# Optimization experiments

Measured on AMD Instinct MI355X. Metric: run time of the kernel, lower is better.

The kernel has to match this reference:

```python
import jax, jax.numpy as jnp
import numpy as np

EMB = 768
HEADS = 12
B, N = 8, 1024


def setup_inputs() -> dict:
    key = jax.random.key(0)
    ks = jax.random.split(key, 5)
    x = jax.random.normal(ks[0], (B, N, EMB), dtype=jnp.float32)
    # torch Linear params expressed as (in, out) matrices: y = x @ W + b
    W_qkv = jax.random.normal(ks[1], (EMB, 3 * EMB), dtype=jnp.float32) * (EMB ** -0.5)
    b_qkv = jax.random.normal(ks[2], (3 * EMB,), dtype=jnp.float32) * 0.02
    W_proj = jax.random.normal(ks[3], (EMB, EMB), dtype=jnp.float32) * (EMB ** -0.5)
    b_proj = jax.random.normal(ks[4], (EMB,), dtype=jnp.float32) * 0.02
    return {"x": x, "W_qkv": W_qkv, "b_qkv": b_qkv, "W_proj": W_proj, "b_proj": b_proj}


def reference(x, W_qkv, b_qkv, W_proj, b_proj):
    b, n, e = x.shape
    h = HEADS
    d = e // h
    qkv = x @ W_qkv + b_qkv                      # (b, n, 3e)
    # rearrange 'b n (h d qkv) -> qkv b h n d': qkv is the INNERMOST factor
    qkv = qkv.reshape(b, n, h, d, 3)
    q = jnp.transpose(qkv[..., 0], (0, 2, 1, 3))  # (b, h, n, d)
    k = jnp.transpose(qkv[..., 1], (0, 2, 1, 3))
    v = jnp.transpose(qkv[..., 2], (0, 2, 1, 3))
    energy = jnp.einsum('bhqd,bhkd->bhqk', q, k)  # UNscaled scores
    # faithful to source: softmax first, THEN divide by sqrt(emb_size)
    att = jax.nn.softmax(energy, axis=-1) / jnp.sqrt(jnp.float32(e))
    out = jnp.einsum('bhql,bhld->bhqd', att, v)   # (b, h, n, d)
    out = jnp.transpose(out, (0, 2, 1, 3)).reshape(b, n, e)
    return out @ W_proj + b_proj
```

## Files before the change

kernel.cpp:

```cpp
#include <hip/hip_runtime.h>
#include <hip/hip_bf16.h>
#include <stdint.h>

#define EMB 768
#define HEADS 12
#define BATCH 8
#define SEQ 1024
#define HD 64
#define M_ROWS (BATCH * SEQ)
#define QKV_COLS (3 * EMB)

typedef __attribute__((ext_vector_type(8))) short short8;
typedef __attribute__((ext_vector_type(4))) float f32x4;

__device__ __forceinline__ unsigned short f2bf(float x) {
    union { float f; unsigned u; } v; v.f = x;
    unsigned r = v.u + 0x7FFFu + ((v.u >> 16) & 1u);
    return (unsigned short)(r >> 16);
}
__device__ __forceinline__ float bf2f(unsigned short h) {
    union { unsigned u; float f; } v; v.u = ((unsigned)h) << 16;
    return v.f;
}
__device__ __forceinline__ float truncbf(float x) {
    return __uint_as_float(__float_as_uint(x) & 0xFFFF0000u);
}
__device__ __forceinline__ uint32_t packtr(float a, float b) {
    return (__float_as_uint(a) >> 16) | (__float_as_uint(b) & 0xFFFF0000u);
}

#define MFMA16(a, b, c) __builtin_amdgcn_mfma_f32_16x16x32_bf16((a), (b), (c), 0, 0, 0)

__global__ __launch_bounds__(256, 2)
void gemm_qkv(const float* __restrict__ X, const float* __restrict__ W,
              const float* __restrict__ bias,
              unsigned short* __restrict__ Qh, unsigned short* __restrict__ Ql,
              unsigned short* __restrict__ Kh, unsigned short* __restrict__ Kl,
              unsigned short* __restrict__ Vt)
{
    __shared__ unsigned short Ash[128][40], Asl[128][40];
    __shared__ unsigned short Bsh[128][40], Bsl[128][40];

    const int tid  = threadIdx.x;
    const int wave = tid >> 6, lane = tid & 63;
    const int lr = lane & 15, lg = lane >> 4;
    const int wr = (wave >> 1) * 64, wc = (wave & 1) * 64;
    const int m0 = blockIdx.y * 128;
    const int c0 = blockIdx.x * 128;

    const f32x4 fzero = {0.f, 0.f, 0.f, 0.f};
    f32x4 acc[4][4];
    #pragma unroll
    for (int m = 0; m < 4; ++m)
        #pragma unroll
        for (int n = 0; n < 4; ++n) acc[m][n] = fzero;

    const int kgB = tid & 7;
    const int cgB = tid >> 3;

    for (int k0 = 0; k0 < EMB; k0 += 32) {
        #pragma unroll
        for (int p = 0; p < 4; ++p) {
            int idx = (p << 8) + tid;
            int row = idx >> 3, kc = (idx & 7) << 2;
            f32x4 v = *reinterpret_cast<const f32x4*>(X + (size_t)(m0 + row) * EMB + k0 + kc);
            float l0 = v[0] - truncbf(v[0]), l1 = v[1] - truncbf(v[1]);
            float l2 = v[2] - truncbf(v[2]), l3 = v[3] - truncbf(v[3]);
            uint2 hw = { packtr(v[0], v[1]), packtr(v[2], v[3]) };
            uint2 lw = { packtr(l0, l1), packtr(l2, l3) };
            *reinterpret_cast<uint2*>(&Ash[row][kc]) = hw;
            *reinterpret_cast<uint2*>(&Asl[row][kc]) = lw;
        }
        {
            f32x4 v[4];
            #pragma unroll
            for (int i = 0; i < 4; ++i)
                v[i] = *reinterpret_cast<const f32x4*>(
                    W + (size_t)(k0 + kgB * 4 + i) * QKV_COLS + c0 + cgB * 4);
            #pragma unroll
            for (int j = 0; j < 4; ++j) {
                float a0 = v[0][j], a1 = v[1][j], a2 = v[2][j], a3 = v[3][j];
                float b0 = a0 - truncbf(a0), b1 = a1 - truncbf(a1);
                float b2 = a2 - truncbf(a2), b3 = a3 - truncbf(a3);
                uint2 hw = { packtr(a0, a1), packtr(a2, a3) };
                uint2 lw = { packtr(b0, b1), packtr(b2, b3) };
                *reinterpret_cast<uint2*>(&Bsh[cgB * 4 + j][kgB * 4]) = hw;
                *reinterpret_cast<uint2*>(&Bsl[cgB * 4 + j][kgB * 4]) = lw;
            }
        }
        __syncthreads();

        short8 ah[4], al[4], bh[4], bl[4];
        #pragma unroll
        for (int m = 0; m < 4; ++m) {
            ah[m] = *reinterpret_cast<const short8*>(&Ash[wr + m * 16 + lr][lg << 3]);
            al[m] = *reinterpret_cast<const short8*>(&Asl[wr + m * 16 + lr][lg << 3]);
        }
        #pragma unroll
        for (int n = 0; n < 4; ++n) {
            bh[n] = *reinterpret_cast<const short8*>(&Bsh[wc + n * 16 + lr][lg << 3]);
            bl[n] = *reinterpret_cast<const short8*>(&Bsl[wc + n * 16 + lr][lg << 3]);
        }
        #pragma unroll
        for (int m = 0; m < 4; ++m)
            #pragma unroll
            for (int n = 0; n < 4; ++n) {
                acc[m][n] = MFMA16(ah[m], bh[n], acc[m][n]);
                acc[m][n] = MFMA16(ah[m], bl[n], acc[m][n]);
                acc[m][n] = MFMA16(al[m], bh[n], acc[m][n]);
            }
        __syncthreads();
    }

    #pragma unroll
    for (int m = 0; m < 4; ++m) {
        #pragma unroll
        for (int n = 0; n < 4; ++n) {
            const int colg = c0 + wc + n * 16 + lr;
            const float bv = bias[colg];
            const int which = colg % 3;
            const int h  = colg / 192;
            const int dd = (colg % 192) / 3;
            const int rowg0 = m0 + wr + m * 16 + (lg << 2);
            const int bi = rowg0 >> 10, ni0 = rowg0 & (SEQ - 1);
            const int bhid = bi * HEADS + h;
            if (which == 2) {
                const float v0 = acc[m][n][0] + bv, v1 = acc[m][n][1] + bv;
                const float v2 = acc[m][n][2] + bv, v3 = acc[m][n][3] + bv;
                uint2 w = { (uint32_t)f2bf(v0) | ((uint32_t)f2bf(v1) << 16),
                            (uint32_t)f2bf(v2) | ((uint32_t)f2bf(v3) << 16) };
                *reinterpret_cast<uint2*>(Vt + ((size_t)bhid * HD + dd) * SEQ + ni0) = w;
            } else {
                unsigned short* __restrict__ Ph = (which == 0) ? Qh : Kh;
                unsigned short* __restrict__ Pl = (which == 0) ? Ql : Kl;
                #pragma unroll
                for (int j = 0; j < 4; ++j) {
                    const float val = acc[m][n][j] + bv;
                    const size_t oidx = ((size_t)bhid * SEQ + ni0 + j) * HD + dd;
                    const uint32_t uv = __float_as_uint(val);
                    Ph[oidx] = (unsigned short)(uv >> 16);
                    Pl[oidx] = (unsigned short)(__float_as_uint(
                        val - __uint_as_float(uv & 0xFFFF0000u)) >> 16);
                }
            }
        }
    }
}

__global__ __launch_bounds__(256, 2)
void attn_fused(const unsigned short* __restrict__ Qh, const unsigned short* __restrict__ Ql,
                const unsigned short* __restrict__ Kh, const unsigned short* __restrict__ Kl,
                const unsigned short* __restrict__ Vt,
                unsigned short* __restrict__ Ob)
{
    __shared__ unsigned short Vs[64][72];
    __shared__ unsigned short Ksh[64][72];
    __shared__ unsigned short Ksl[64][72];
    __shared__ unsigned short Plds[4][16][72];

    const int tid  = threadIdx.x;
    const int wave = tid >> 6, lane = tid & 63;
    const int lr = lane & 15, lg = lane >> 4;

    const int bid = blockIdx.x;
    const int lid = (bid & 7) * 192 + (bid >> 3);
    const int qt = lid & 15;
    const int bh = lid >> 4;
    const int b = bh / HEADS, h = bh % HEADS;

    const size_t base = (size_t)bh * SEQ * HD;
    const unsigned short* Qhb = Qh + base;
    const unsigned short* Qlb = Ql + base;
    const unsigned short* Khb = Kh + base;
    const unsigned short* Klb = Kl + base;
    const unsigned short* Vtb = Vt + base;

    const int q0 = qt * 64 + wave * 16;

    short8 qh[2], ql[2];
    #pragma unroll
    for (int kk = 0; kk < 2; ++kk) {
        const size_t off = (size_t)(q0 + lr) * HD + kk * 32 + (lg << 3);
        qh[kk] = *reinterpret_cast<const short8*>(Qhb + off);
        ql[kk] = *reinterpret_cast<const short8*>(Qlb + off);
    }

    float m = -1.0e30f, l = 0.f;
    f32x4 oacc[4];
    const f32x4 fzero = {0.f, 0.f, 0.f, 0.f};
    #pragma unroll
    for (int d = 0; d < 4; ++d) oacc[d] = fzero;

    for (int t = 0; t < SEQ / 64; ++t) {
        const int kbase = t * 64;

        __syncthreads();
        #pragma unroll
        for (int p = 0; p < 2; ++p) {
            int idx = (p << 8) + tid;
            int r = idx >> 3, c = (idx & 7) << 3;
            *reinterpret_cast<uint4*>(&Vs[r][c]) =
                *reinterpret_cast<const uint4*>(Vtb + (size_t)r * SEQ + kbase + c);
            *reinterpret_cast<uint4*>(&Ksh[r][c]) =
                *reinterpret_cast<const uint4*>(Khb + (size_t)(kbase + r) * HD + c);
            *reinterpret_cast<uint4*>(&Ksl[r][c]) =
                *reinterpret_cast<const uint4*>(Klb + (size_t)(kbase + r) * HD + c);
        }
        __syncthreads();

        f32x4 s[4];
        #pragma unroll
        for (int n = 0; n < 4; ++n) s[n] = fzero;
        #pragma unroll
        for (int n = 0; n < 4; ++n) {
            #pragma unroll
            for (int kk = 0; kk < 2; ++kk) {
                const short8 kh = *reinterpret_cast<const short8*>(&Ksh[n * 16 + lr][kk * 32 + (lg << 3)]);
                const short8 kl = *reinterpret_cast<const short8*>(&Ksl[n * 16 + lr][kk * 32 + (lg << 3)]);
                s[n] = MFMA16(kh, qh[kk], s[n]);
                s[n] = MFMA16(kh, ql[kk], s[n]);
                s[n] = MFMA16(kl, qh[kk], s[n]);
            }
        }

        float t0 = fmaxf(fmaxf(s[0][0], s[0][1]), fmaxf(s[0][2], s[0][3]));
        float t1 = fmaxf(fmaxf(s[1][0], s[1][1]), fmaxf(s[1][2], s[1][3]));
        float t2 = fmaxf(fmaxf(s[2][0], s[2][1]), fmaxf(s[2][2], s[2][3]));
        float t3 = fmaxf(fmaxf(s[3][0], s[3][1]), fmaxf(s[3][2], s[3][3]));
        float tmax = fmaxf(fmaxf(t0, t1), fmaxf(t2, t3));
        tmax = fmaxf(tmax, __shfl_xor(tmax, 16));
        tmax = fmaxf(tmax, __shfl_xor(tmax, 32));

        const float mnew = fmaxf(m, tmax);
        const float corr = __expf(m - mnew);
        m = mnew;

        float psum = 0.f;
        #pragma unroll
        for (int n = 0; n < 4; ++n) {
            const float p0 = __expf(s[n][0] - mnew), p1 = __expf(s[n][1] - mnew);
            const float p2 = __expf(s[n][2] - mnew), p3 = __expf(s[n][3] - mnew);
            psum += (p0 + p1) + (p2 + p3);
            uint2 w = { (uint32_t)f2bf(p0) | ((uint32_t)f2bf(p1) << 16),
                        (uint32_t)f2bf(p2) | ((uint32_t)f2bf(p3) << 16) };
            *reinterpret_cast<uint2*>(&Plds[wave][lr][n * 16 + (lg << 2)]) = w;
        }
        psum += __shfl_xor(psum, 16);
        psum += __shfl_xor(psum, 32);
        l = l * corr + psum;

        #pragma unroll
        for (int j = 0; j < 4; ++j) {
            const float cj = __shfl(corr, (lg << 2) + j);
            oacc[0][j] *= cj; oacc[1][j] *= cj;
            oacc[2][j] *= cj; oacc[3][j] *= cj;
        }

        #pragma unroll
        for (int kk = 0; kk < 2; ++kk) {
            const short8 ap = *reinterpret_cast<const short8*>(&Plds[wave][lr][kk * 32 + (lg << 3)]);
            #pragma unroll
            for (int d = 0; d < 4; ++d) {
                const short8 bv = *reinterpret_cast<const short8*>(&Vs[d * 16 + lr][kk * 32 + (lg << 3)]);
                oacc[d] = MFMA16(ap, bv, oacc[d]);
            }
        }
    }

    const float rs = 0.036084391824351615f;
    #pragma unroll
    for (int j = 0; j < 4; ++j) {
        const float lj = __shfl(l, (lg << 2) + j);
        const float sc = rs / lj;
        const int q = q0 + (lg << 2) + j;
        #pragma unroll
        for (int d = 0; d < 4; ++d) {
            const float val = oacc[d][j] * sc;
            Ob[((size_t)b * SEQ + q) * EMB + h * HD + d * 16 + lr] = f2bf(val);
        }
    }
}

__global__ __launch_bounds__(256, 2)
void gemm_proj(const unsigned short* __restrict__ A, const float* __restrict__ W,
               const float* __restrict__ bias, float* __restrict__ Out)
{
    __shared__ unsigned short As[128][40];
    __shared__ unsigned short Bs[128][40];

    const int tid  = threadIdx.x;
    const int wave = tid >> 6, lane = tid & 63;
    const int lr = lane & 15, lg = lane >> 4;
    const int wr = (wave >> 1) * 64, wc = (wave & 1) * 64;
    const int m0 = blockIdx.y * 128;
    const int c0 = blockIdx.x * 128;

    const f32x4 fzero = {0.f, 0.f, 0.f, 0.f};
    f32x4 acc[4][4];
    #pragma unroll
    for (int m = 0; m < 4; ++m)
        #pragma unroll
        for (int n = 0; n < 4; ++n) acc[m][n] = fzero;

    const int kgB = tid & 7, cgB = tid >> 3;

    for (int k0 = 0; k0 < EMB; k0 += 32) {
        #pragma unroll
        for (int p = 0; p < 2; ++p) {
            int idx = (p << 8) + tid;
            int row = idx >> 2, kc = (idx & 3) << 3;
            uint4 v = *reinterpret_cast<const uint4*>(A + (size_t)(m0 + row) * EMB + k0 + kc);
            *reinterpret_cast<uint4*>(&As[row][kc]) = v;
        }
        {
            f32x4 v[4];
            #pragma unroll
            for (int i = 0; i < 4; ++i)
                v[i] = *reinterpret_cast<const f32x4*>(
                    W + (size_t)(k0 + kgB * 4 + i) * EMB + c0 + cgB * 4);
            #pragma unroll
            for (int j = 0; j < 4; ++j) {
                uint2 w = { (uint32_t)f2bf(v[0][j]) | ((uint32_t)f2bf(v[1][j]) << 16),
                            (uint32_t)f2bf(v[2][j]) | ((uint32_t)f2bf(v[3][j]) << 16) };
                *reinterpret_cast<uint2*>(&Bs[cgB * 4 + j][kgB * 4]) = w;
            }
        }
        __syncthreads();

        short8 a[4], b[4];
        #pragma unroll
        for (int m = 0; m < 4; ++m)
            a[m] = *reinterpret_cast<const short8*>(&As[wr + m * 16 + lr][lg << 3]);
        #pragma unroll
        for (int n = 0; n < 4; ++n)
            b[n] = *reinterpret_cast<const short8*>(&Bs[wc + n * 16 + lr][lg << 3]);
        #pragma unroll
        for (int m = 0; m < 4; ++m)
            #pragma unroll
            for (int n = 0; n < 4; ++n)
                acc[m][n] = MFMA16(a[m], b[n], acc[m][n]);
        __syncthreads();
    }

    #pragma unroll
    for (int m = 0; m < 4; ++m) {
        #pragma unroll
        for (int n = 0; n < 4; ++n) {
            const int colg = c0 + wc + n * 16 + lr;
            const float bv = bias[colg];
            #pragma unroll
            for (int j = 0; j < 4; ++j) {
                const int rowg = m0 + wr + m * 16 + (lg << 2) + j;
                Out[(size_t)rowg * EMB + colg] = acc[m][n][j] + bv;
            }
        }
    }
}

extern "C" void kernel_launch(void* const* d_in, const int* in_sizes, int n_in,
                              void* d_out, int out_size, void* d_ws, size_t ws_size,
                              hipStream_t stream)
{
    const float* x     = (const float*)d_in[0];
    const float* Wqkv  = (const float*)d_in[1];
    const float* bqkv  = (const float*)d_in[2];
    const float* Wproj = (const float*)d_in[3];
    const float* bproj = (const float*)d_in[4];
    float* out = (float*)d_out;

    const size_t NQ = (size_t)BATCH * HEADS * SEQ * HD;
    unsigned short* Qh = (unsigned short*)d_ws;
    unsigned short* Ql = Qh + NQ;
    unsigned short* Kh = Ql + NQ;
    unsigned short* Kl = Kh + NQ;
    unsigned short* Vt = Kl + NQ;
    unsigned short* Ob = Vt + NQ;

    gemm_qkv<<<dim3(QKV_COLS / 128, M_ROWS / 128), 256, 0, stream>>>(
        x, Wqkv, bqkv, Qh, Ql, Kh, Kl, Vt);
    attn_fused<<<dim3(16 * BATCH * HEADS), 256, 0, stream>>>(Qh, Ql, Kh, Kl, Vt, Ob);
    gemm_proj<<<dim3(EMB / 128, M_ROWS / 128), 256, 0, stream>>>(
        Ob, Wproj, bproj, out);
}
```

Before: 244.1 us.

## Presplit X and transpose-split W into bf16 hi/lo before QKV GEMM

Adds two prepass kernels: one splits X into bf16 high/low halves, the other splits W_qkv and transposes it into column-major bf16 high/low buffers. The QKV GEMM then loads ready-made bf16 tiles with 16-byte copies instead of converting fp32 per tile, and its occupancy hint rises from 2 to 4 blocks per CU. This removes conversion work that was repeated for every output tile and the strided W loads. The cost is two extra launches plus a write and re-read of the split buffers, stored in the output buffer and the attention workspace.

```diff
diff --git a/kernel.cpp b/kernel.cpp
--- a/kernel.cpp
+++ b/kernel.cpp
@@ -31,8 +31,59 @@
 
 #define MFMA16(a, b, c) __builtin_amdgcn_mfma_f32_16x16x32_bf16((a), (b), (c), 0, 0, 0)
 
-__global__ __launch_bounds__(256, 2)
-void gemm_qkv(const float* __restrict__ X, const float* __restrict__ W,
+__global__ __launch_bounds__(256)
+void split_x(const float* __restrict__ X,
+             unsigned short* __restrict__ Xh, unsigned short* __restrict__ Xl)
+{
+    const size_t i = ((size_t)blockIdx.x * 256 + threadIdx.x) * 8;
+    f32x4 a = *reinterpret_cast<const f32x4*>(X + i);
+    f32x4 b = *reinterpret_cast<const f32x4*>(X + i + 4);
+    uint4 hw = { packtr(a[0], a[1]), packtr(a[2], a[3]),
+                 packtr(b[0], b[1]), packtr(b[2], b[3]) };
+    float l0 = a[0] - truncbf(a[0]), l1 = a[1] - truncbf(a[1]);
+    float l2 = a[2] - truncbf(a[2]), l3 = a[3] - truncbf(a[3]);
+    float l4 = b[0] - truncbf(b[0]), l5 = b[1] - truncbf(b[1]);
+    float l6 = b[2] - truncbf(b[2]), l7 = b[3] - truncbf(b[3]);
+    uint4 lw = { packtr(l0, l1), packtr(l2, l3), packtr(l4, l5), packtr(l6, l7) };
+    *reinterpret_cast<uint4*>(Xh + i) = hw;
+    *reinterpret_cast<uint4*>(Xl + i) = lw;
+}
+
+__global__ __launch_bounds__(256)
+void split_tw(const float* __restrict__ W,
+              unsigned short* __restrict__ Wht, unsigned short* __restrict__ Wlt)
+{
+    __shared__ unsigned short Th[64][72], Tl[64][72];
+    const int tid = threadIdx.x;
+    const int ct = blockIdx.x * 64;
+    const int kt = blockIdx.y * 64;
+
+    #pragma unroll
+    for (int p = 0; p < 4; ++p) {
+        int idx = (p << 8) + tid;
+        int k = idx >> 4, c4 = (idx & 15) << 2;
+        f32x4 v = *reinterpret_cast<const f32x4*>(W + (size_t)(kt + k) * QKV_COLS + ct + c4);
+        #pragma unroll
+        for (int j = 0; j < 4; ++j) {
+            Th[c4 + j][k] = (unsigned short)(__float_as_uint(v[j]) >> 16);
+            Tl[c4 + j][k] = (unsigned short)(__float_as_uint(v[j] - truncbf(v[j])) >> 16);
+        }
+    }
+    __syncthreads();
+    #pragma unroll
+    for (int p = 0; p < 2; ++p) {
+        int idx = (p << 8) + tid;
+        int c = idx >> 3, k8 = (idx & 7) << 3;
+        *reinterpret_cast<uint4*>(Wht + (size_t)(ct + c) * EMB + kt + k8) =
+            *reinterpret_cast<const uint4*>(&Th[c][k8]);
+        *reinterpret_cast<uint4*>(Wlt + (size_t)(ct + c) * EMB + kt + k8) =
+            *reinterpret_cast<const uint4*>(&Tl[c][k8]);
+    }
+}
+
+__global__ __launch_bounds__(256, 4)
+void gemm_qkv(const unsigned short* __restrict__ Xh, const unsigned short* __restrict__ Xl,
+              const unsigned short* __restrict__ Wht, const unsigned short* __restrict__ Wlt,
               const float* __restrict__ bias,
               unsigned short* __restrict__ Qh, unsigned short* __restrict__ Ql,
               unsigned short* __restrict__ Kh, unsigned short* __restrict__ Kl,
@@ -55,38 +106,17 @@
         #pragma unroll
         for (int n = 0; n < 4; ++n) acc[m][n] = fzero;
 
-    const int kgB = tid & 7;
-    const int cgB = tid >> 3;
-
     for (int k0 = 0; k0 < EMB; k0 += 32) {
         #pragma unroll
-        for (int p = 0; p < 4; ++p) {
+        for (int p = 0; p < 2; ++p) {
             int idx = (p << 8) + tid;
-            int row = idx >> 3, kc = (idx & 7) << 2;
-            f32x4 v = *reinterpret_cast<const f32x4*>(X + (size_t)(m0 + row) * EMB + k0 + kc);
-            float l0 = v[0] - truncbf(v[0]), l1 = v[1] - truncbf(v[1]);
-            float l2 = v[2] - truncbf(v[2]), l3 = v[3] - truncbf(v[3]);
-            uint2 hw = { packtr(v[0], v[1]), packtr(v[2], v[3]) };
-            uint2 lw = { packtr(l0, l1), packtr(l2, l3) };
-            *reinterpret_cast<uint2*>(&Ash[row][kc]) = hw;
-            *reinterpret_cast<uint2*>(&Asl[row][kc]) = lw;
-        }
-        {
-            f32x4 v[4];
-            #pragma unroll
-            for (int i = 0; i < 4; ++i)
-                v[i] = *reinterpret_cast<const f32x4*>(
-                    W + (size_t)(k0 + kgB * 4 + i) * QKV_COLS + c0 + cgB * 4);
-            #pragma unroll
-            for (int j = 0; j < 4; ++j) {
-                float a0 = v[0][j], a1 = v[1][j], a2 = v[2][j], a3 = v[3][j];
-                float b0 = a0 - truncbf(a0), b1 = a1 - truncbf(a1);
-                float b2 = a2 - truncbf(a2), b3 = a3 - truncbf(a3);
-                uint2 hw = { packtr(a0, a1), packtr(a2, a3) };
-                uint2 lw = { packtr(b0, b1), packtr(b2, b3) };
-                *reinterpret_cast<uint2*>(&Bsh[cgB * 4 + j][kgB * 4]) = hw;
-                *reinterpret_cast<uint2*>(&Bsl[cgB * 4 + j][kgB * 4]) = lw;
-            }
+            int row = idx >> 2, kc = (idx & 3) << 3;
+            const size_t aoff = (size_t)(m0 + row) * EMB + k0 + kc;
+            const size_t boff = (size_t)(c0 + row) * EMB + k0 + kc;
+            *reinterpret_cast<uint4*>(&Ash[row][kc]) = *reinterpret_cast<const uint4*>(Xh + aoff);
+            *reinterpret_cast<uint4*>(&Asl[row][kc]) = *reinterpret_cast<const uint4*>(Xl + aoff);
+            *reinterpret_cast<uint4*>(&Bsh[row][kc]) = *reinterpret_cast<const uint4*>(Wht + boff);
+            *reinterpret_cast<uint4*>(&Bsl[row][kc]) = *reinterpret_cast<const uint4*>(Wlt + boff);
         }
         __syncthreads();
 
@@ -369,6 +399,9 @@
     float* out = (float*)d_out;
 
     const size_t NQ = (size_t)BATCH * HEADS * SEQ * HD;
+    const size_t NX = (size_t)M_ROWS * EMB;
+    const size_t NW = (size_t)EMB * QKV_COLS;
+
     unsigned short* Qh = (unsigned short*)d_ws;
     unsigned short* Ql = Qh + NQ;
     unsigned short* Kh = Ql + NQ;
@@ -376,8 +409,15 @@
     unsigned short* Vt = Kl + NQ;
     unsigned short* Ob = Vt + NQ;
 
+    unsigned short* Xh  = (unsigned short*)d_out;
+    unsigned short* Xl  = Xh + NX;
+    unsigned short* Wht = Ob;
+    unsigned short* Wlt = Wht + NW;
+
+    split_x<<<dim3(NX / 8 / 256), 256, 0, stream>>>(x, Xh, Xl);
+    split_tw<<<dim3(QKV_COLS / 64, EMB / 64), 256, 0, stream>>>(Wqkv, Wht, Wlt);
     gemm_qkv<<<dim3(QKV_COLS / 128, M_ROWS / 128), 256, 0, stream>>>(
-        x, Wqkv, bqkv, Qh, Ql, Kh, Kl, Vt);
+        Xh, Xl, Wht, Wlt, bqkv, Qh, Ql, Kh, Kl, Vt);
     attn_fused<<<dim3(16 * BATCH * HEADS), 256, 0, stream>>>(Qh, Ql, Kh, Kl, Vt, Ob);
     gemm_proj<<<dim3(EMB / 128, M_ROWS / 128), 256, 0, stream>>>(
         Ob, Wproj, bproj, out);
```

Measured after the change: 276.7 us. +13.3%, slower.
